# Kernel optimization log

Hardware: AMD Instinct MI355X
Metric: run time of the kernel (lower is better)

Reference implementation:

```python
import jax, jax.numpy as jnp
import numpy as np
import math

NH = 12      # num attention heads
WIN = 128    # one-sided sliding window
NG = 32      # number of global (prefix) tokens
NEG = -1e9
LN_EPS = 1e-12


def _layernorm(x, g, b):
    mu = jnp.mean(x, axis=-1, keepdims=True)
    var = jnp.mean(jnp.square(x - mu), axis=-1, keepdims=True)
    return (x - mu) * jax.lax.rsqrt(var + LN_EPS) * g + b


def _longformer_self_attn(h, am, Wq, bq, Wk, bk, Wv, bv):
    B, S, D = h.shape
    Dh = D // NH
    w = WIN
    C = S // w  # number of chunks

    def proj(Wm, bm):
        return (h @ Wm + bm).reshape(B, S, NH, Dh).transpose(0, 2, 1, 3)

    q = proj(Wq, bq) * (1.0 / math.sqrt(Dh))  # [B,H,S,Dh]
    k = proj(Wk, bk)
    v = proj(Wv, bv)

    # ---- banded (sliding window) scores, chunked: each query chunk sees 3w keys ----
    kp = jnp.pad(k, ((0, 0), (0, 0), (w, w), (0, 0)))
    vp = jnp.pad(v, ((0, 0), (0, 0), (w, w), (0, 0)))
    idx = jnp.arange(C)[:, None] * w + jnp.arange(3 * w)[None, :]  # [C,3w]
    k3 = kp[:, :, idx]  # [B,H,C,3w,Dh]
    v3 = vp[:, :, idx]
    qc = q.reshape(B, NH, C, w, Dh)
    band = jnp.einsum('bhcqd,bhckd->bhcqk', qc, k3)  # [B,H,C,w,3w]

    qpos = (jnp.arange(C) * w)[:, None, None] + jnp.arange(w)[None, :, None]  # [C,w,1]
    kpos = (idx - w)[:, None, :]  # [C,1,3w] absolute key positions
    valid = (jnp.abs(kpos - qpos) <= w) & (kpos >= NG) & (kpos < S)  # band, exclude global keys

    amp = jnp.pad(am, ((0, 0), (w, w)))
    am3 = amp[:, idx]  # [B,C,3w] additive mask gathered per chunk
    band = band + am3[:, None, :, None, :]
    band = jnp.where(valid[None, None], band, NEG)
    band = band.reshape(B, NH, S, 3 * w)

    # ---- every token also attends to the NG global tokens ----
    gsc = jnp.einsum('bhsd,bhgd->bhsg', q, k[:, :, :NG]) + am[:, None, None, :NG]

    logits = jnp.concatenate([band, gsc], axis=-1)  # [B,H,S,3w+NG]
    probs = jax.nn.softmax(logits, axis=-1)
    pb = probs[..., :3 * w].reshape(B, NH, C, w, 3 * w)
    out = jnp.einsum('bhcqk,bhckd->bhcqd', pb, v3).reshape(B, NH, S, Dh)
    out = out + jnp.einsum('bhsg,bhgd->bhsd', probs[..., 3 * w:], v[:, :, :NG])

    # ---- global tokens attend to everything ----
    gl = jnp.einsum('bhgd,bhsd->bhgs', q[:, :, :NG], k) + am[:, None, None, :]
    outg = jnp.einsum('bhgs,bhsd->bhgd', jax.nn.softmax(gl, axis=-1), v)

    ctx = jnp.concatenate([outg, out[:, :, NG:]], axis=2)  # [B,H,S,Dh]
    return ctx.transpose(0, 2, 1, 3).reshape(B, S, D)


def setup_inputs() -> dict:
    key = jax.random.key(0)
    ks = jax.random.split(key, 8)
    B, S, D, F = 2, 4096, 768, 3072
    p = lambda k_, sh: jax.random.normal(k_, sh, jnp.float32) * 0.02
    return {
        'hidden_states': jax.random.normal(ks[0], (B, S, D), jnp.float32),
        'attention_mask': jnp.zeros((B, S), jnp.float32),
        'Wq': p(ks[1], (D, D)), 'bq': jnp.zeros((D,), jnp.float32),
        'Wk': p(ks[2], (D, D)), 'bk': jnp.zeros((D,), jnp.float32),
        'Wv': p(ks[3], (D, D)), 'bv': jnp.zeros((D,), jnp.float32),
        'Wo': p(ks[4], (D, D)), 'bo': jnp.zeros((D,), jnp.float32),
        'ln1_g': jnp.ones((D,), jnp.float32), 'ln1_b': jnp.zeros((D,), jnp.float32),
        'Wi': p(ks[5], (D, F)), 'bi': jnp.zeros((F,), jnp.float32),
        'Wo2': p(ks[6], (F, D)), 'bo2': jnp.zeros((D,), jnp.float32),
        'ln2_g': jnp.ones((D,), jnp.float32), 'ln2_b': jnp.zeros((D,), jnp.float32),
    }


def reference(hidden_states, attention_mask, Wq, bq, Wk, bk, Wv, bv, Wo, bo,
              ln1_g, ln1_b, Wi, bi, Wo2, bo2, ln2_g, ln2_b):
    ctx = _longformer_self_attn(hidden_states, attention_mask, Wq, bq, Wk, bk, Wv, bv)
    attn_out = _layernorm(ctx @ Wo + bo + hidden_states, ln1_g, ln1_b)
    inter = jax.nn.gelu(attn_out @ Wi + bi, approximate=False)
    layer_out = _layernorm(inter @ Wo2 + bo2 + attn_out, ln2_g, ln2_b)
    return layer_out
```

## Files before the change

kernel.cpp:

```cpp
#include <hip/hip_runtime.h>
#include <math.h>

#define NHEAD 12
#define DH 64
#define S_LEN 4096
#define B_SZ 2
#define D_MODEL 768
#define FF_DIM 3072
#define WINSZ 128
#define NGLB 32
#define NEGV -1e9f
#define NQC 6291456L

typedef __attribute__((ext_vector_type(8))) short bf16x8;
typedef __attribute__((ext_vector_type(4))) float floatx4;

__device__ __forceinline__ unsigned short f2bf(float x) {
    union { float f; unsigned u; } v; v.f = x;
    unsigned r = v.u + 0x7fffu + ((v.u >> 16) & 1u);
    return (unsigned short)(r >> 16);
}
__device__ __forceinline__ float bf2f(unsigned short x) {
    union { unsigned u; float f; } v; v.u = ((unsigned)x) << 16;
    return v.f;
}

__device__ __forceinline__ void async_copy16(const unsigned short* g, unsigned short* l) {
    __builtin_amdgcn_global_load_lds(
        (const __attribute__((address_space(1))) void*)g,
        (__attribute__((address_space(3))) void*)l, 16, 0, 0);
}

__global__ __launch_bounds__(256) void conv_k(
    const float* __restrict__ x, unsigned short* __restrict__ y, long n)
{
    long i = ((long)blockIdx.x * 256 + threadIdx.x) * 4;
    if (i >= n) return;
    float4 v = *(const float4*)(x + i);
    ushort4 o;
    o.x = f2bf(v.x); o.y = f2bf(v.y); o.z = f2bf(v.z); o.w = f2bf(v.w);
    *(ushort4*)(y + i) = o;
}

__global__ __launch_bounds__(256) void bcat_k(
    const float* __restrict__ a, const float* __restrict__ b,
    const float* __restrict__ c, float* __restrict__ o)
{
    int i = blockIdx.x * 256 + threadIdx.x;
    if (i < 768) o[i] = a[i];
    else if (i < 1536) o[i] = b[i - 768];
    else if (i < 2304) o[i] = c[i - 1536];
}

__global__ __launch_bounds__(256) void transpose_k(
    const float* __restrict__ W, unsigned short* __restrict__ WT, int K, int N)
{
    __shared__ float tile[32][33];
    const int tx = threadIdx.x, ty = threadIdx.y;
    const int n0 = blockIdx.x * 32, k0 = blockIdx.y * 32;
#pragma unroll
    for (int i = 0; i < 4; ++i)
        tile[ty + 8 * i][tx] = W[(long)(k0 + ty + 8 * i) * N + n0 + tx];
    __syncthreads();
#pragma unroll
    for (int i = 0; i < 4; ++i)
        WT[(long)(n0 + ty + 8 * i) * K + k0 + tx] = f2bf(tile[tx][ty + 8 * i]);
}

__global__ __launch_bounds__(256) void vt_k(
    const unsigned short* __restrict__ v, unsigned short* __restrict__ vt)
{
    const int bh = blockIdx.y;
    const int s0 = blockIdx.x * 32;
    const int w = threadIdx.x >> 6, lane = threadIdx.x & 63;
    const unsigned short* src = v + ((long)bh * S_LEN + s0 + w * 8) * DH + lane;
    unsigned short r[8];
#pragma unroll
    for (int j = 0; j < 8; ++j) r[j] = src[j * DH];
    unsigned short* dst = vt + ((long)bh * DH + lane) * S_LEN + s0 + w * 8;
    ushort4 lo, hi;
    lo.x = r[0]; lo.y = r[1]; lo.z = r[2]; lo.w = r[3];
    hi.x = r[4]; hi.y = r[5]; hi.z = r[6]; hi.w = r[7];
    *(ushort4*)dst = lo;
    *(ushort4*)(dst + 4) = hi;
}

template <int EPI>
__global__ __launch_bounds__(256) void gemm_bf(
    const unsigned short* __restrict__ A, const unsigned short* __restrict__ BT,
    const float* __restrict__ bias, void* __restrict__ out,
    int M, int N, int K, int nx)
{
    __shared__ unsigned short As[128 * 32];
    __shared__ unsigned short Bs[128 * 32];
    const int tid = threadIdx.x;
    const int wave = tid >> 6, lane = tid & 63;
    const int t8 = (blockIdx.x & 7) * (gridDim.x >> 3) + (blockIdx.x >> 3);
    const int m0 = (t8 / nx) * 128, n0 = (t8 % nx) * 128;
    const int wr = (wave >> 1) * 64, wc = (wave & 1) * 64;

    floatx4 acc[4][4];
#pragma unroll
    for (int i = 0; i < 4; ++i)
#pragma unroll
        for (int j = 0; j < 4; ++j) acc[i][j] = (floatx4){0.f, 0.f, 0.f, 0.f};

    const int srow = lane >> 2;
    const int schk = (((lane & 3) ^ (srow & 3))) * 8;
    const int r = lane & 15;
    const int q8 = ((lane >> 4) ^ (lane & 3)) * 8;

    for (int k0 = 0; k0 < K; k0 += 32) {
#pragma unroll
        for (int gi = 0; gi < 2; ++gi) {
            const int g = wave * 2 + gi;
            async_copy16(A + (long)(m0 + g * 16 + srow) * K + k0 + schk, &As[g * 512]);
            async_copy16(BT + (long)(n0 + g * 16 + srow) * K + k0 + schk, &Bs[g * 512]);
        }
        __syncthreads();

        bf16x8 af[4], bfr[4];
#pragma unroll
        for (int i = 0; i < 4; ++i) {
            af[i]  = *(const bf16x8*)&As[(wr + i * 16 + r) * 32 + q8];
            bfr[i] = *(const bf16x8*)&Bs[(wc + i * 16 + r) * 32 + q8];
        }
#pragma unroll
        for (int i = 0; i < 4; ++i)
#pragma unroll
            for (int j = 0; j < 4; ++j)
                acc[i][j] = __builtin_amdgcn_mfma_f32_16x16x32_bf16(
                    af[i], bfr[j], acc[i][j], 0, 0, 0);
        __syncthreads();
    }

    const int col_l = lane & 15, row_l = (lane >> 4) * 4;
#pragma unroll
    for (int i = 0; i < 4; ++i) {
#pragma unroll
        for (int j = 0; j < 4; ++j) {
            const int n = n0 + wc + j * 16 + col_l;
            const float bv = bias[n];
#pragma unroll
            for (int rg = 0; rg < 4; ++rg) {
                const int m = m0 + wr + i * 16 + row_l + rg;
                float v = acc[i][j][rg] + bv;
                if (EPI == 1) {
                    v = 0.5f * v * (1.f + erff(v * 0.70710678118654752f));
                    ((unsigned short*)out)[(long)m * N + n] = f2bf(v);
                } else {
                    const int bb = m >> 12, s = m & 4095;
                    const int part = n / 768;
                    const int nn = n - part * 768;
                    const int hh = nn >> 6, dh = nn & 63;
                    const float sc = (part == 0) ? 0.125f : 1.f;
                    ((unsigned short*)out)[(long)part * NQC +
                        (((long)bb * NHEAD + hh) * S_LEN + s) * DH + dh] = f2bf(v * sc);
                }
            }
        }
    }
}

__global__ __launch_bounds__(256) void gemm_sp(
    const unsigned short* __restrict__ A, const unsigned short* __restrict__ BT,
    float* __restrict__ p0, float* __restrict__ p1,
    int M, int N, int K2, int nx, int ntile)
{
    __shared__ unsigned short As[128 * 32];
    __shared__ unsigned short Bs[128 * 32];
    const int tid = threadIdx.x;
    const int wave = tid >> 6, lane = tid & 63;
    const int t8 = (blockIdx.x & 7) * (gridDim.x >> 3) + (blockIdx.x >> 3);
    const int slice = t8 >= ntile;
    const int tile = t8 - slice * ntile;
    const int m0 = (tile / nx) * 128, n0 = (tile % nx) * 128;
    const int kbeg = slice * K2, kend = kbeg + K2;
    float* P = slice ? p1 : p0;
    const int wr = (wave >> 1) * 64, wc = (wave & 1) * 64;

    floatx4 acc[4][4];
#pragma unroll
    for (int i = 0; i < 4; ++i)
#pragma unroll
        for (int j = 0; j < 4; ++j) acc[i][j] = (floatx4){0.f, 0.f, 0.f, 0.f};

    const int srow = lane >> 2;
    const int schk = (((lane & 3) ^ (srow & 3))) * 8;
    const int r = lane & 15;
    const int q8 = ((lane >> 4) ^ (lane & 3)) * 8;
    const long Kl = (long)K2 * 2;

    for (int k0 = kbeg; k0 < kend; k0 += 32) {
#pragma unroll
        for (int gi = 0; gi < 2; ++gi) {
            const int g = wave * 2 + gi;
            async_copy16(A + (long)(m0 + g * 16 + srow) * Kl + k0 + schk, &As[g * 512]);
            async_copy16(BT + (long)(n0 + g * 16 + srow) * Kl + k0 + schk, &Bs[g * 512]);
        }
        __syncthreads();

        bf16x8 af[4], bfr[4];
#pragma unroll
        for (int i = 0; i < 4; ++i) {
            af[i]  = *(const bf16x8*)&As[(wr + i * 16 + r) * 32 + q8];
            bfr[i] = *(const bf16x8*)&Bs[(wc + i * 16 + r) * 32 + q8];
        }
#pragma unroll
        for (int i = 0; i < 4; ++i)
#pragma unroll
            for (int j = 0; j < 4; ++j)
                acc[i][j] = __builtin_amdgcn_mfma_f32_16x16x32_bf16(
                    af[i], bfr[j], acc[i][j], 0, 0, 0);
        __syncthreads();
    }

    const int col_l = lane & 15, row_l = (lane >> 4) * 4;
#pragma unroll
    for (int i = 0; i < 4; ++i)
#pragma unroll
        for (int j = 0; j < 4; ++j) {
            const int n = n0 + wc + j * 16 + col_l;
#pragma unroll
            for (int rg = 0; rg < 4; ++rg) {
                const int m = m0 + wr + i * 16 + row_l + rg;
                P[(long)m * N + n] = acc[i][j][rg];
            }
        }
}

__global__ __launch_bounds__(256) void band_mfma_k(
    const unsigned short* __restrict__ q, const unsigned short* __restrict__ k,
    const unsigned short* __restrict__ vt, const float* __restrict__ am,
    unsigned short* __restrict__ ctx)
{
    __shared__ unsigned short Ks[32 * 72];
    __shared__ unsigned short Vs[64 * 40];
    __shared__ unsigned short Ps[4][32 * 40];

    const int blk = blockIdx.x;
    const int c = blk & 31;
    const int h = (blk >> 5) % NHEAD;
    const int b = blk / (32 * NHEAD);
    const int tid = threadIdx.x;
    const int wave = tid >> 6, lane = tid & 63;
    const long bh = (long)b * NHEAD + h;

    const unsigned short* kh  = k + bh * S_LEN * DH;
    const unsigned short* vth = vt + bh * (long)DH * S_LEN;
    const float* amb = am + (long)b * S_LEN;

    const int q0 = c * WINSZ + wave * 32;
    const int ln15 = lane & 15, ln4 = lane >> 4;

    bf16x8 qf[2][2];
#pragma unroll
    for (int nt = 0; nt < 2; ++nt)
#pragma unroll
        for (int ks = 0; ks < 2; ++ks)
            qf[nt][ks] = *(const bf16x8*)(q + (bh * S_LEN + q0 + nt * 16 + ln15) * DH
                                          + ks * 32 + ln4 * 8);

    floatx4 o[4][2];
#pragma unroll
    for (int mt = 0; mt < 4; ++mt)
#pragma unroll
        for (int nt = 0; nt < 2; ++nt) o[mt][nt] = (floatx4){0.f, 0.f, 0.f, 0.f};
    float m_r[2] = {-1e30f, -1e30f}, l_r[2] = {0.f, 0.f};

    const int sk_key = tid >> 3, sk_ch = tid & 7;
    const int sv_dim = tid & 63, sv_ch = tid >> 6;
    const bf16x8 zero8 = {0, 0, 0, 0, 0, 0, 0, 0};

    for (int tile = 0; tile < 13; ++tile) {
        const bool glob = (tile == 12);
        const int kbase = glob ? 0 : (c * WINSZ - WINSZ + tile * 32);

        __syncthreads();
        {
            int kpos = kbase + sk_key;
            bf16x8 val = zero8;
            if ((unsigned)kpos < (unsigned)S_LEN)
                val = *(const bf16x8*)(kh + (long)kpos * DH + sk_ch * 8);
            *(bf16x8*)(&Ks[sk_key * 72 + sk_ch * 8]) = val;
        }
        {
            int kc = kbase + sv_ch * 8;
            bf16x8 val = zero8;
            if (kc >= 0 && kc + 8 <= S_LEN)
                val = *(const bf16x8*)(vth + (long)sv_dim * S_LEN + kc);
            *(bf16x8*)(&Vs[sv_dim * 40 + sv_ch * 8]) = val;
        }
        __syncthreads();

        bf16x8 ak[2][2];
#pragma unroll
        for (int mt = 0; mt < 2; ++mt)
#pragma unroll
            for (int ks = 0; ks < 2; ++ks)
                ak[mt][ks] = *(const bf16x8*)(&Ks[(mt * 16 + ln15) * 72 + ks * 32 + ln4 * 8]);

        floatx4 s[2][2];
#pragma unroll
        for (int mt = 0; mt < 2; ++mt)
#pragma unroll
            for (int nt = 0; nt < 2; ++nt) {
                floatx4 acc = (floatx4){0.f, 0.f, 0.f, 0.f};
                acc = __builtin_amdgcn_mfma_f32_16x16x32_bf16(ak[mt][0], qf[nt][0], acc, 0, 0, 0);
                acc = __builtin_amdgcn_mfma_f32_16x16x32_bf16(ak[mt][1], qf[nt][1], acc, 0, 0, 0);
                s[mt][nt] = acc;
            }

#pragma unroll
        for (int mt = 0; mt < 2; ++mt) {
            const int kp0 = kbase + mt * 16 + ln4 * 4;
#pragma unroll
            for (int rg = 0; rg < 4; ++rg) {
                const int kpos = kp0 + rg;
                const bool kin = (unsigned)kpos < (unsigned)S_LEN;
                const float amv = kin ? amb[kpos] : 0.f;
#pragma unroll
                for (int nt = 0; nt < 2; ++nt) {
                    const int qpos = q0 + nt * 16 + ln15;
                    const int dlt = kpos > qpos ? kpos - qpos : qpos - kpos;
                    const bool valid = glob || (kpos >= NGLB && kin && dlt <= WINSZ);
                    s[mt][nt][rg] = valid ? s[mt][nt][rg] + amv : NEGV;
                }
            }
        }

        float alpha[2];
#pragma unroll
        for (int nt = 0; nt < 2; ++nt) {
            float mx = s[0][nt][0];
#pragma unroll
            for (int rg = 1; rg < 4; ++rg) mx = fmaxf(mx, s[0][nt][rg]);
#pragma unroll
            for (int rg = 0; rg < 4; ++rg) mx = fmaxf(mx, s[1][nt][rg]);
            mx = fmaxf(mx, __shfl_xor(mx, 16));
            mx = fmaxf(mx, __shfl_xor(mx, 32));
            const float mn = fmaxf(m_r[nt], mx);
            alpha[nt] = __expf(m_r[nt] - mn);
            m_r[nt] = mn;
        }

#pragma unroll
        for (int nt = 0; nt < 2; ++nt) {
            float sum = 0.f;
#pragma unroll
            for (int mt = 0; mt < 2; ++mt) {
                ushort4 pk;
#pragma unroll
                for (int rg = 0; rg < 4; ++rg) {
                    const float p = __expf(s[mt][nt][rg] - m_r[nt]);
                    sum += p;
                    ((unsigned short*)&pk)[rg] = f2bf(p);
                }
                *(ushort4*)(&Ps[wave][(nt * 16 + ln15) * 40 + mt * 16 + ln4 * 4]) = pk;
            }
            sum += __shfl_xor(sum, 16);
            sum += __shfl_xor(sum, 32);
            l_r[nt] = l_r[nt] * alpha[nt] + sum;
        }

#pragma unroll
        for (int mt = 0; mt < 4; ++mt)
#pragma unroll
            for (int nt = 0; nt < 2; ++nt)
#pragma unroll
                for (int rg = 0; rg < 4; ++rg) o[mt][nt][rg] *= alpha[nt];

        bf16x8 av[4], bp[2];
#pragma unroll
        for (int mt = 0; mt < 4; ++mt)
            av[mt] = *(const bf16x8*)(&Vs[(mt * 16 + ln15) * 40 + ln4 * 8]);
#pragma unroll
        for (int nt = 0; nt < 2; ++nt)
            bp[nt] = *(const bf16x8*)(&Ps[wave][(nt * 16 + ln15) * 40 + ln4 * 8]);
#pragma unroll
        for (int mt = 0; mt < 4; ++mt)
#pragma unroll
            for (int nt = 0; nt < 2; ++nt)
                o[mt][nt] = __builtin_amdgcn_mfma_f32_16x16x32_bf16(
                    av[mt], bp[nt], o[mt][nt], 0, 0, 0);
    }

    const float inv0 = 1.f / l_r[0], inv1 = 1.f / l_r[1];
#pragma unroll
    for (int nt = 0; nt < 2; ++nt) {
        const float inv = nt ? inv1 : inv0;
        const long row = (long)b * S_LEN + q0 + nt * 16 + ln15;
#pragma unroll
        for (int mt = 0; mt < 4; ++mt) {
            ushort4 ov;
#pragma unroll
            for (int rg = 0; rg < 4; ++rg)
                ((unsigned short*)&ov)[rg] = f2bf(o[mt][nt][rg] * inv);
            *(ushort4*)(ctx + row * D_MODEL + h * DH + mt * 16 + ln4 * 4) = ov;
        }
    }
}

__global__ __launch_bounds__(512) void glob_mfma_k(
    const unsigned short* __restrict__ q, const unsigned short* __restrict__ k,
    const unsigned short* __restrict__ vt, const float* __restrict__ am,
    unsigned short* __restrict__ ctx)
{
    __shared__ unsigned short Ps[8][32 * 72];
    __shared__ float Om[64 * 36];
    __shared__ float mW[8][32], lW[8][32], lTot[32];

    const int bh = blockIdx.x;
    const int b = bh / NHEAD, h = bh % NHEAD;
    const int tid = threadIdx.x;
    const int wave = tid >> 6, lane = tid & 63;
    const int ln15 = lane & 15, ln4 = lane >> 4;

    const unsigned short* kh  = k + (long)bh * S_LEN * DH;
    const unsigned short* vth = vt + (long)bh * DH * S_LEN;
    const float* amb = am + (long)b * S_LEN;

    bf16x8 qf[2][2];
#pragma unroll
    for (int nt = 0; nt < 2; ++nt)
#pragma unroll
        for (int ks = 0; ks < 2; ++ks)
            qf[nt][ks] = *(const bf16x8*)(q + ((long)bh * S_LEN + nt * 16 + ln15) * DH
                                          + ks * 32 + ln4 * 8);

    floatx4 o[4][2];
#pragma unroll
    for (int mt = 0; mt < 4; ++mt)
#pragma unroll
        for (int nt = 0; nt < 2; ++nt) o[mt][nt] = (floatx4){0.f, 0.f, 0.f, 0.f};
    float m_r[2] = {-1e30f, -1e30f}, l_r[2] = {0.f, 0.f};

    for (int it = 0; it < 8; ++it) {
        const int kbase = it * 512 + wave * 64;

        bf16x8 ak[4][2];
#pragma unroll
        for (int mt = 0; mt < 4; ++mt)
#pragma unroll
            for (int ks = 0; ks < 2; ++ks)
                ak[mt][ks] = *(const bf16x8*)(kh + (long)(kbase + mt * 16 + ln15) * DH
                                              + ks * 32 + ln4 * 8);

        floatx4 s[4][2];
#pragma unroll
        for (int mt = 0; mt < 4; ++mt)
#pragma unroll
            for (int nt = 0; nt < 2; ++nt) {
                floatx4 acc = (floatx4){0.f, 0.f, 0.f, 0.f};
                acc = __builtin_amdgcn_mfma_f32_16x16x32_bf16(ak[mt][0], qf[nt][0], acc, 0, 0, 0);
                acc = __builtin_amdgcn_mfma_f32_16x16x32_bf16(ak[mt][1], qf[nt][1], acc, 0, 0, 0);
                s[mt][nt] = acc;
            }

#pragma unroll
        for (int mt = 0; mt < 4; ++mt) {
            const int kp0 = kbase + mt * 16 + ln4 * 4;
#pragma unroll
            for (int rg = 0; rg < 4; ++rg) {
                const float amv = amb[kp0 + rg];
#pragma unroll
                for (int nt = 0; nt < 2; ++nt) s[mt][nt][rg] += amv;
            }
        }

        float alpha[2];
#pragma unroll
        for (int nt = 0; nt < 2; ++nt) {
            float mx = s[0][nt][0];
#pragma unroll
            for (int mt = 0; mt < 4; ++mt)
#pragma unroll
                for (int rg = 0; rg < 4; ++rg) mx = fmaxf(mx, s[mt][nt][rg]);
            mx = fmaxf(mx, __shfl_xor(mx, 16));
            mx = fmaxf(mx, __shfl_xor(mx, 32));
            const float mn = fmaxf(m_r[nt], mx);
            alpha[nt] = __expf(m_r[nt] - mn);
            m_r[nt] = mn;
        }

#pragma unroll
        for (int nt = 0; nt < 2; ++nt) {
            float sum = 0.f;
#pragma unroll
            for (int mt = 0; mt < 4; ++mt) {
                ushort4 pk;
#pragma unroll
                for (int rg = 0; rg < 4; ++rg) {
                    const float p = __expf(s[mt][nt][rg] - m_r[nt]);
                    sum += p;
                    ((unsigned short*)&pk)[rg] = f2bf(p);
                }
                *(ushort4*)(&Ps[wave][(nt * 16 + ln15) * 72 + mt * 16 + ln4 * 4]) = pk;
            }
            sum += __shfl_xor(sum, 16);
            sum += __shfl_xor(sum, 32);
            l_r[nt] = l_r[nt] * alpha[nt] + sum;
        }

#pragma unroll
        for (int mt = 0; mt < 4; ++mt)
#pragma unroll
            for (int nt = 0; nt < 2; ++nt)
#pragma unroll
                for (int rg = 0; rg < 4; ++rg) o[mt][nt][rg] *= alpha[nt];

        bf16x8 av[4][2], bp[2][2];
#pragma unroll
        for (int mt = 0; mt < 4; ++mt)
#pragma unroll
            for (int ks = 0; ks < 2; ++ks)
                av[mt][ks] = *(const bf16x8*)(vth + (long)(mt * 16 + ln15) * S_LEN
                                              + kbase + ks * 32 + ln4 * 8);
#pragma unroll
        for (int nt = 0; nt < 2; ++nt)
#pragma unroll
            for (int ks = 0; ks < 2; ++ks)
                bp[nt][ks] = *(const bf16x8*)(&Ps[wave][(nt * 16 + ln15) * 72
                                              + ks * 32 + ln4 * 8]);
#pragma unroll
        for (int mt = 0; mt < 4; ++mt)
#pragma unroll
            for (int nt = 0; nt < 2; ++nt) {
                o[mt][nt] = __builtin_amdgcn_mfma_f32_16x16x32_bf16(
                    av[mt][0], bp[nt][0], o[mt][nt], 0, 0, 0);
                o[mt][nt] = __builtin_amdgcn_mfma_f32_16x16x32_bf16(
                    av[mt][1], bp[nt][1], o[mt][nt], 0, 0, 0);
            }
    }

    if (ln4 == 0) {
#pragma unroll
        for (int nt = 0; nt < 2; ++nt) {
            mW[wave][nt * 16 + ln15] = m_r[nt];
            lW[wave][nt * 16 + ln15] = l_r[nt];
        }
    }
    for (int i = tid; i < 64 * 36; i += 512) Om[i] = 0.f;
    __syncthreads();

    float f[2];
#pragma unroll
    for (int nt = 0; nt < 2; ++nt) {
        const int qq = nt * 16 + ln15;
        float mt_ = mW[0][qq];
#pragma unroll
        for (int w = 1; w < 8; ++w) mt_ = fmaxf(mt_, mW[w][qq]);
        float lt = 0.f;
#pragma unroll
        for (int w = 0; w < 8; ++w) lt += __expf(mW[w][qq] - mt_) * lW[w][qq];
        f[nt] = __expf(m_r[nt] - mt_);
        if (wave == 0 && ln4 == 0) lTot[qq] = lt;
    }
#pragma unroll
    for (int mt = 0; mt < 4; ++mt)
#pragma unroll
        for (int nt = 0; nt < 2; ++nt)
#pragma unroll
            for (int rg = 0; rg < 4; ++rg) o[mt][nt][rg] *= f[nt];

    for (int wv = 0; wv < 8; ++wv) {
        if (wave == wv) {
#pragma unroll
            for (int mt = 0; mt < 4; ++mt)
#pragma unroll
                for (int nt = 0; nt < 2; ++nt)
#pragma unroll
                    for (int rg = 0; rg < 4; ++rg)
                        Om[(mt * 16 + ln4 * 4 + rg) * 36 + nt * 16 + ln15] += o[mt][nt][rg];
        }
        __syncthreads();
    }

    const int qq = tid >> 4, d0 = (tid & 15) * 4;
    const float inv = 1.f / lTot[qq];
    ushort4 ov;
#pragma unroll
    for (int i = 0; i < 4; ++i)
        ((unsigned short*)&ov)[i] = f2bf(Om[(d0 + i) * 36 + qq] * inv);
    *(ushort4*)(ctx + ((long)b * S_LEN + qq) * D_MODEL + h * DH + d0) = ov;
}

__global__ __launch_bounds__(256) void ln2p_k(
    const float* __restrict__ p0, const float* __restrict__ p1,
    const float* __restrict__ bias, const float* __restrict__ resid,
    float* __restrict__ out, unsigned short* __restrict__ out_bf,
    const float* __restrict__ gw, const float* __restrict__ bw)
{
    __shared__ float red[256];
    const long row = blockIdx.x;
    const long base = row * D_MODEL;
    const int t = threadIdx.x;
    float v0 = p0[base + t]       + p1[base + t]       + bias[t]       + resid[base + t];
    float v1 = p0[base + t + 256] + p1[base + t + 256] + bias[t + 256] + resid[base + t + 256];
    float v2 = p0[base + t + 512] + p1[base + t + 512] + bias[t + 512] + resid[base + t + 512];

    red[t] = v0 + v1 + v2;
    __syncthreads();
    for (int off = 128; off; off >>= 1) {
        if (t < off) red[t] += red[t + off];
        __syncthreads();
    }
    const float mu = red[0] * (1.f / 768.f);
    __syncthreads();

    float d0 = v0 - mu, d1 = v1 - mu, d2 = v2 - mu;
    red[t] = d0 * d0 + d1 * d1 + d2 * d2;
    __syncthreads();
    for (int off = 128; off; off >>= 1) {
        if (t < off) red[t] += red[t + off];
        __syncthreads();
    }
    const float var = red[0] * (1.f / 768.f);
    const float rs = rsqrtf(var + 1e-12f);

    const float y0 = d0 * rs * gw[t] + bw[t];
    const float y1 = d1 * rs * gw[t + 256] + bw[t + 256];
    const float y2 = d2 * rs * gw[t + 512] + bw[t + 512];
    if (out) {
        float* y = out + base;
        y[t] = y0; y[t + 256] = y1; y[t + 512] = y2;
    }
    if (out_bf) {
        unsigned short* yb = out_bf + base;
        yb[t] = f2bf(y0); yb[t + 256] = f2bf(y1); yb[t + 512] = f2bf(y2);
    }
}

extern "C" void kernel_launch(void* const* d_in, const int* in_sizes, int n_in,
                              void* d_out, int out_size, void* d_ws, size_t ws_size,
                              hipStream_t stream)
{
    const float* hid  = (const float*)d_in[0];
    const float* am   = (const float*)d_in[1];
    const float* Wq   = (const float*)d_in[2];
    const float* bq   = (const float*)d_in[3];
    const float* Wk   = (const float*)d_in[4];
    const float* bk   = (const float*)d_in[5];
    const float* Wv   = (const float*)d_in[6];
    const float* bv   = (const float*)d_in[7];
    const float* Wo   = (const float*)d_in[8];
    const float* bo   = (const float*)d_in[9];
    const float* ln1g = (const float*)d_in[10];
    const float* ln1b = (const float*)d_in[11];
    const float* Wi   = (const float*)d_in[12];
    const float* bi   = (const float*)d_in[13];
    const float* Wo2  = (const float*)d_in[14];
    const float* bo2  = (const float*)d_in[15];
    const float* ln2g = (const float*)d_in[16];
    const float* ln2b = (const float*)d_in[17];

    const long M  = (long)B_SZ * S_LEN;
    const long NQ = NQC;

    unsigned short* W16 = (unsigned short*)d_ws;
    unsigned short* qb   = W16;
    unsigned short* kb   = W16 + NQ;
    unsigned short* vb   = W16 + 2 * NQ;
    unsigned short* vtb  = W16 + 3 * NQ;
    unsigned short* ctxb = W16 + 4 * NQ;
    unsigned short* hidb = W16 + 5 * NQ;
    unsigned short* wqt  = W16 + 6 * NQ;
    unsigned short* wkt  = wqt + 589824;
    unsigned short* wvt  = wkt + 589824;
    unsigned short* wot  = wvt + 589824;
    unsigned short* wit  = wot + 589824;
    unsigned short* wo2t = wit + 2359296;
    float* tmp   = (float*)(W16 + 44826624);
    float* partB1 = (float*)(W16 + 57409536);
    float* bcat  = (float*)(W16 + 69992448);
    float* partA0 = (float*)W16;
    float* partA1 = (float*)(W16 + 2 * NQ);
    unsigned short* interb = W16;
    unsigned short* attnb  = hidb;
    float* partB0 = (float*)(W16 + 4 * NQ);
    (void)ws_size; (void)in_sizes; (void)n_in; (void)out_size;

    transpose_k<<<dim3(24, 24), dim3(32, 8), 0, stream>>>(Wq, wqt, 768, 768);
    transpose_k<<<dim3(24, 24), dim3(32, 8), 0, stream>>>(Wk, wkt, 768, 768);
    transpose_k<<<dim3(24, 24), dim3(32, 8), 0, stream>>>(Wv, wvt, 768, 768);
    transpose_k<<<dim3(24, 24), dim3(32, 8), 0, stream>>>(Wo, wot, 768, 768);
    transpose_k<<<dim3(96, 24), dim3(32, 8), 0, stream>>>(Wi, wit, 768, 3072);
    transpose_k<<<dim3(24, 96), dim3(32, 8), 0, stream>>>(Wo2, wo2t, 3072, 768);
    conv_k<<<dim3((NQ / 4 + 255) / 256), dim3(256), 0, stream>>>(hid, hidb, NQ);
    bcat_k<<<dim3(9), dim3(256), 0, stream>>>(bq, bk, bv, bcat);

    dim3 blk(256);

    gemm_bf<2><<<dim3(1152), blk, 0, stream>>>(hidb, wqt, bcat, qb,
                                               M, 2304, 768, 18);

    vt_k<<<dim3(128, 24), blk, 0, stream>>>(vb, vtb);

    band_mfma_k<<<dim3(768), blk, 0, stream>>>(qb, kb, vtb, am, ctxb);
    glob_mfma_k<<<dim3(B_SZ * NHEAD), dim3(512), 0, stream>>>(qb, kb, vtb, am, ctxb);

    gemm_sp<<<dim3(768), blk, 0, stream>>>(ctxb, wot, partA0, partA1,
                                           M, 768, 384, 6, 384);
    ln2p_k<<<dim3(M), blk, 0, stream>>>(partA0, partA1, bo, hid,
                                        tmp, attnb, ln1g, ln1b);

    gemm_bf<1><<<dim3(1536), blk, 0, stream>>>(attnb, wit, bi, interb,
                                               M, 3072, 768, 24);

    gemm_sp<<<dim3(768), blk, 0, stream>>>(interb, wo2t, partB0, partB1,
                                           M, 768, 1536, 6, 384);
    ln2p_k<<<dim3(M), blk, 0, stream>>>(partB0, partB1, bo2, tmp,
                                        (float*)d_out, nullptr, ln2g, ln2b);
}
```

Measured before the change: 462.9 us.

## Replace GEMMs with 256x256-tile 8-wave double-buffered pipelined MFMA kernel

Replaces the 128x128, single-buffered 4-wave GEMM kernels (gemm_bf and gemm_sp) with one templated 512-thread kernel. It computes 256x256 tiles with a K step of 64 and double-buffers shared memory, issuing async copies for the next tile while MFMA runs. It also adds explicit barriers, waitcnt, sched_barrier and setprio scheduling. The aim is more data reuse per tile and latency hiding in the QKV, output, FFN1 and FFN2 GEMMs. In exchange, 128KB of LDS and large accumulators limit occupancy, and grids become small (192-384 blocks), which risks poor CU utilization on 256 CUs.

```diff
diff --git a/kernel.cpp b/kernel.cpp
--- a/kernel.cpp
+++ b/kernel.cpp
@@ -85,148 +85,188 @@
     *(ushort4*)(dst + 4) = hi;
 }
 
+#define MFMA_QUAD(MM, NN, BREG)                                                \
+    __builtin_amdgcn_s_setprio(1);                                             \
+    _Pragma("unroll")                                                          \
+    for (int f = 0; f < 4; ++f)                                                \
+        _Pragma("unroll")                                                      \
+        for (int g = 0; g < 2; ++g)                                            \
+            _Pragma("unroll")                                                  \
+            for (int ks = 0; ks < 2; ++ks)                                     \
+                acc[(MM) * 4 + f][(NN) * 2 + g] =                              \
+                    __builtin_amdgcn_mfma_f32_16x16x32_bf16(                   \
+                        af[f][ks], BREG[g][ks], acc[(MM) * 4 + f][(NN) * 2 + g], 0, 0, 0); \
+    __builtin_amdgcn_s_setprio(0);
+
 template <int EPI>
-__global__ __launch_bounds__(256) void gemm_bf(
+__global__ __launch_bounds__(512, 2) void gemm8(
     const unsigned short* __restrict__ A, const unsigned short* __restrict__ BT,
-    const float* __restrict__ bias, void* __restrict__ out,
-    int M, int N, int K, int nx)
-{
-    __shared__ unsigned short As[128 * 32];
-    __shared__ unsigned short Bs[128 * 32];
+    const float* __restrict__ bias, void* __restrict__ out, float* __restrict__ out1,
+    int M, int N, int Kst, int K2, int nx, int ntile)
+{
+    __shared__ __align__(16) unsigned short As[32768];
+    __shared__ __align__(16) unsigned short Bs[32768];
+
     const int tid = threadIdx.x;
-    const int wave = tid >> 6, lane = tid & 63;
-    const int t8 = (blockIdx.x & 7) * (gridDim.x >> 3) + (blockIdx.x >> 3);
-    const int m0 = (t8 / nx) * 128, n0 = (t8 % nx) * 128;
-    const int wr = (wave >> 1) * 64, wc = (wave & 1) * 64;
-
-    floatx4 acc[4][4];
-#pragma unroll
-    for (int i = 0; i < 4; ++i)
+    const int w = tid >> 6, lane = tid & 63;
+    int t8 = (blockIdx.x & 7) * (gridDim.x >> 3) + (blockIdx.x >> 3);
+    int kbeg = 0;
+    float* P = (float*)out;
+    if (EPI == 0) {
+        if (t8 >= ntile) { t8 -= ntile; kbeg = K2; P = out1; }
+    }
+    const int m0 = (t8 / nx) * 256, n0 = (t8 % nx) * 256;
+    const int NT = K2 >> 6;
+
+    const int wr = w >> 2, wc = w & 3;
+    const int ln15 = lane & 15, ln4 = lane >> 4;
+    const int wr8 = wr << 3, wc4 = wc << 2;
+
+    const int srow = lane >> 2;
+    const int scol = ((lane & 3) << 3) ^ ((lane & 32) >> 1);
+    const int ruA = w * 16 + srow;
+    const int rA0 = ((ruA >> 6) << 7) + (ruA & 63);
+    const int rB0 = ((ruA >> 5) << 6) + (ruA & 31);
+    const unsigned short* gA[2];
+    const unsigned short* gB[2];
+    gA[0] = A + (long)(m0 + rA0) * Kst + kbeg + scol;
+    gA[1] = A + (long)(m0 + rA0 + 64) * Kst + kbeg + scol;
+    gB[0] = BT + (long)(n0 + rB0) * Kst + kbeg + scol;
+    gB[1] = BT + (long)(n0 + rB0 + 32) * Kst + kbeg + scol;
+    const int wld = w << 10;
+
+    auto issueA = [&](int mu, int tt) {
+        const unsigned short* g = gA[mu] + (long)tt * 64;
+        unsigned short* l = &As[((((tt & 1) << 1) | mu) << 13) + wld];
+        async_copy16(g, l);
+        async_copy16(g + 32, l + 512);
+    };
+    auto issueB = [&](int nu, int tt) {
+        const unsigned short* g = gB[nu] + (long)tt * 64;
+        unsigned short* l = &Bs[((((tt & 1) << 1) | nu) << 13) + wld];
+        async_copy16(g, l);
+        async_copy16(g + 32, l + 512);
+    };
+
+    const int p2 = ((ln15 << 5) | (ln4 << 3)) ^ ((ln15 & 8) << 1);
+
+    floatx4 acc[8][4];
+#pragma unroll
+    for (int i = 0; i < 8; ++i)
 #pragma unroll
         for (int j = 0; j < 4; ++j) acc[i][j] = (floatx4){0.f, 0.f, 0.f, 0.f};
-
-    const int srow = lane >> 2;
-    const int schk = (((lane & 3) ^ (srow & 3))) * 8;
-    const int r = lane & 15;
-    const int q8 = ((lane >> 4) ^ (lane & 3)) * 8;
-
-    for (int k0 = 0; k0 < K; k0 += 32) {
-#pragma unroll
-        for (int gi = 0; gi < 2; ++gi) {
-            const int g = wave * 2 + gi;
-            async_copy16(A + (long)(m0 + g * 16 + srow) * K + k0 + schk, &As[g * 512]);
-            async_copy16(BT + (long)(n0 + g * 16 + srow) * K + k0 + schk, &Bs[g * 512]);
-        }
-        __syncthreads();
-
-        bf16x8 af[4], bfr[4];
-#pragma unroll
-        for (int i = 0; i < 4; ++i) {
-            af[i]  = *(const bf16x8*)&As[(wr + i * 16 + r) * 32 + q8];
-            bfr[i] = *(const bf16x8*)&Bs[(wc + i * 16 + r) * 32 + q8];
-        }
-#pragma unroll
-        for (int i = 0; i < 4; ++i)
-#pragma unroll
-            for (int j = 0; j < 4; ++j)
-                acc[i][j] = __builtin_amdgcn_mfma_f32_16x16x32_bf16(
-                    af[i], bfr[j], acc[i][j], 0, 0, 0);
-        __syncthreads();
-    }
-
-    const int col_l = lane & 15, row_l = (lane >> 4) * 4;
-#pragma unroll
-    for (int i = 0; i < 4; ++i) {
-#pragma unroll
-        for (int j = 0; j < 4; ++j) {
-            const int n = n0 + wc + j * 16 + col_l;
-            const float bv = bias[n];
-#pragma unroll
-            for (int rg = 0; rg < 4; ++rg) {
-                const int m = m0 + wr + i * 16 + row_l + rg;
-                float v = acc[i][j][rg] + bv;
-                if (EPI == 1) {
+    bf16x8 af[4][2], b0[2][2], b1[2][2];
+
+    issueA(0, 0); issueB(0, 0); issueA(1, 0); issueB(1, 0);
+    if (NT > 1) {
+        issueA(0, 1); issueB(0, 1);
+        asm volatile("s_waitcnt vmcnt(4)" ::: "memory");
+    } else {
+        asm volatile("s_waitcnt vmcnt(0)" ::: "memory");
+    }
+    __builtin_amdgcn_s_barrier();
+    __builtin_amdgcn_sched_barrier(0);
+
+    for (int u = 0; u < NT; ++u) {
+        const unsigned short* Ab = &As[((u & 1) << 14) + p2];
+        const unsigned short* Bb = &Bs[((u & 1) << 14) + p2];
+
+#pragma unroll
+        for (int f = 0; f < 4; ++f)
+#pragma unroll
+            for (int ks = 0; ks < 2; ++ks)
+                af[f][ks] = *(const bf16x8*)(Ab + ((wr8 + f * 2 + ks) << 9));
+#pragma unroll
+        for (int g = 0; g < 2; ++g)
+#pragma unroll
+            for (int ks = 0; ks < 2; ++ks)
+                b0[g][ks] = *(const bf16x8*)(Bb + ((wc4 + g * 2 + ks) << 9));
+        if (u + 1 < NT) issueA(1, u + 1);
+        __builtin_amdgcn_sched_barrier(0);
+        __builtin_amdgcn_s_barrier();
+        asm volatile("s_waitcnt lgkmcnt(0)" ::: "memory");
+        __builtin_amdgcn_sched_barrier(0);
+        MFMA_QUAD(0, 0, b0)
+        __builtin_amdgcn_sched_barrier(0);
+        __builtin_amdgcn_s_barrier();
+
+#pragma unroll
+        for (int g = 0; g < 2; ++g)
+#pragma unroll
+            for (int ks = 0; ks < 2; ++ks)
+                b1[g][ks] = *(const bf16x8*)(Bb + 8192 + ((wc4 + g * 2 + ks) << 9));
+        if (u + 1 < NT) issueB(1, u + 1);
+        __builtin_amdgcn_sched_barrier(0);
+        __builtin_amdgcn_s_barrier();
+        asm volatile("s_waitcnt lgkmcnt(0)" ::: "memory");
+        __builtin_amdgcn_sched_barrier(0);
+        MFMA_QUAD(0, 1, b1)
+        __builtin_amdgcn_sched_barrier(0);
+        __builtin_amdgcn_s_barrier();
+
+#pragma unroll
+        for (int f = 0; f < 4; ++f)
+#pragma unroll
+            for (int ks = 0; ks < 2; ++ks)
+                af[f][ks] = *(const bf16x8*)(Ab + 8192 + ((wr8 + f * 2 + ks) << 9));
+        if (u + 2 < NT) issueA(0, u + 2);
+        __builtin_amdgcn_sched_barrier(0);
+        __builtin_amdgcn_s_barrier();
+        asm volatile("s_waitcnt lgkmcnt(0)" ::: "memory");
+        __builtin_amdgcn_sched_barrier(0);
+        MFMA_QUAD(1, 0, b0)
+        __builtin_amdgcn_sched_barrier(0);
+        __builtin_amdgcn_s_barrier();
+
+        if (u + 2 < NT) issueB(0, u + 2);
+        __builtin_amdgcn_sched_barrier(0);
+        __builtin_amdgcn_s_barrier();
+        asm volatile("s_waitcnt lgkmcnt(0)" ::: "memory");
+        __builtin_amdgcn_sched_barrier(0);
+        MFMA_QUAD(1, 1, b1)
+        __builtin_amdgcn_sched_barrier(0);
+        if (u + 2 < NT)      asm volatile("s_waitcnt vmcnt(4)" ::: "memory");
+        else if (u + 1 < NT) asm volatile("s_waitcnt vmcnt(0)" ::: "memory");
+        __builtin_amdgcn_s_barrier();
+        __builtin_amdgcn_sched_barrier(0);
+    }
+
+    const int col_l = lane & 15, row_l = ln4 << 2;
+#pragma unroll
+    for (int mi = 0; mi < 8; ++mi) {
+        const int mbase = m0 + wr * 128 + ((mi >> 2) << 6) + ((mi & 3) << 4) + row_l;
+#pragma unroll
+        for (int ni = 0; ni < 4; ++ni) {
+            const int n = n0 + wc * 64 + ((ni >> 1) << 5) + ((ni & 1) << 4) + col_l;
+            if (EPI == 0) {
+#pragma unroll
+                for (int rg = 0; rg < 4; ++rg)
+                    P[(long)(mbase + rg) * N + n] = acc[mi][ni][rg];
+            } else if (EPI == 1) {
+                const float bv = bias[n];
+#pragma unroll
+                for (int rg = 0; rg < 4; ++rg) {
+                    float v = acc[mi][ni][rg] + bv;
                     v = 0.5f * v * (1.f + erff(v * 0.70710678118654752f));
-                    ((unsigned short*)out)[(long)m * N + n] = f2bf(v);
-                } else {
+                    ((unsigned short*)out)[(long)(mbase + rg) * N + n] = f2bf(v);
+                }
+            } else {
+                const float bv = bias[n];
+                const int part = n / 768;
+                const int nn = n - part * 768;
+                const int hh = nn >> 6, dh = nn & 63;
+                const float sc = (part == 0) ? 0.125f : 1.f;
+#pragma unroll
+                for (int rg = 0; rg < 4; ++rg) {
+                    const int m = mbase + rg;
                     const int bb = m >> 12, s = m & 4095;
-                    const int part = n / 768;
-                    const int nn = n - part * 768;
-                    const int hh = nn >> 6, dh = nn & 63;
-                    const float sc = (part == 0) ? 0.125f : 1.f;
                     ((unsigned short*)out)[(long)part * NQC +
-                        (((long)bb * NHEAD + hh) * S_LEN + s) * DH + dh] = f2bf(v * sc);
+                        (((long)bb * NHEAD + hh) * S_LEN + s) * DH + dh] =
+                        f2bf((acc[mi][ni][rg] + bv) * sc);
                 }
             }
         }
     }
-}
-
-__global__ __launch_bounds__(256) void gemm_sp(
-    const unsigned short* __restrict__ A, const unsigned short* __restrict__ BT,
-    float* __restrict__ p0, float* __restrict__ p1,
-    int M, int N, int K2, int nx, int ntile)
-{
-    __shared__ unsigned short As[128 * 32];
-    __shared__ unsigned short Bs[128 * 32];
-    const int tid = threadIdx.x;
-    const int wave = tid >> 6, lane = tid & 63;
-    const int t8 = (blockIdx.x & 7) * (gridDim.x >> 3) + (blockIdx.x >> 3);
-    const int slice = t8 >= ntile;
-    const int tile = t8 - slice * ntile;
-    const int m0 = (tile / nx) * 128, n0 = (tile % nx) * 128;
-    const int kbeg = slice * K2, kend = kbeg + K2;
-    float* P = slice ? p1 : p0;
-    const int wr = (wave >> 1) * 64, wc = (wave & 1) * 64;
-
-    floatx4 acc[4][4];
-#pragma unroll
-    for (int i = 0; i < 4; ++i)
-#pragma unroll
-        for (int j = 0; j < 4; ++j) acc[i][j] = (floatx4){0.f, 0.f, 0.f, 0.f};
-
-    const int srow = lane >> 2;
-    const int schk = (((lane & 3) ^ (srow & 3))) * 8;
-    const int r = lane & 15;
-    const int q8 = ((lane >> 4) ^ (lane & 3)) * 8;
-    const long Kl = (long)K2 * 2;
-
-    for (int k0 = kbeg; k0 < kend; k0 += 32) {
-#pragma unroll
-        for (int gi = 0; gi < 2; ++gi) {
-            const int g = wave * 2 + gi;
-            async_copy16(A + (long)(m0 + g * 16 + srow) * Kl + k0 + schk, &As[g * 512]);
-            async_copy16(BT + (long)(n0 + g * 16 + srow) * Kl + k0 + schk, &Bs[g * 512]);
-        }
-        __syncthreads();
-
-        bf16x8 af[4], bfr[4];
-#pragma unroll
-        for (int i = 0; i < 4; ++i) {
-            af[i]  = *(const bf16x8*)&As[(wr + i * 16 + r) * 32 + q8];
-            bfr[i] = *(const bf16x8*)&Bs[(wc + i * 16 + r) * 32 + q8];
-        }
-#pragma unroll
-        for (int i = 0; i < 4; ++i)
-#pragma unroll
-            for (int j = 0; j < 4; ++j)
-                acc[i][j] = __builtin_amdgcn_mfma_f32_16x16x32_bf16(
-                    af[i], bfr[j], acc[i][j], 0, 0, 0);
-        __syncthreads();
-    }
-
-    const int col_l = lane & 15, row_l = (lane >> 4) * 4;
-#pragma unroll
-    for (int i = 0; i < 4; ++i)
-#pragma unroll
-        for (int j = 0; j < 4; ++j) {
-            const int n = n0 + wc + j * 16 + col_l;
-#pragma unroll
-            for (int rg = 0; rg < 4; ++rg) {
-                const int m = m0 + wr + i * 16 + row_l + rg;
-                P[(long)m * N + n] = acc[i][j][rg];
-            }
-        }
 }
 
 __global__ __launch_bounds__(256) void band_mfma_k(
@@ -689,26 +729,24 @@
     conv_k<<<dim3((NQ / 4 + 255) / 256), dim3(256), 0, stream>>>(hid, hidb, NQ);
     bcat_k<<<dim3(9), dim3(256), 0, stream>>>(bq, bk, bv, bcat);
 
-    dim3 blk(256);
-
-    gemm_bf<2><<<dim3(1152), blk, 0, stream>>>(hidb, wqt, bcat, qb,
-                                               M, 2304, 768, 18);
-
-    vt_k<<<dim3(128, 24), blk, 0, stream>>>(vb, vtb);
-
-    band_mfma_k<<<dim3(768), blk, 0, stream>>>(qb, kb, vtb, am, ctxb);
+    gemm8<2><<<dim3(288), dim3(512), 0, stream>>>(hidb, wqt, bcat, qb, nullptr,
+                                                  (int)M, 2304, 768, 768, 9, 0);
+
+    vt_k<<<dim3(128, 24), dim3(256), 0, stream>>>(vb, vtb);
+
+    band_mfma_k<<<dim3(768), dim3(256), 0, stream>>>(qb, kb, vtb, am, ctxb);
     glob_mfma_k<<<dim3(B_SZ * NHEAD), dim3(512), 0, stream>>>(qb, kb, vtb, am, ctxb);
 
-    gemm_sp<<<dim3(768), blk, 0, stream>>>(ctxb, wot, partA0, partA1,
-                                           M, 768, 384, 6, 384);
-    ln2p_k<<<dim3(M), blk, 0, stream>>>(partA0, partA1, bo, hid,
-                                        tmp, attnb, ln1g, ln1b);
-
-    gemm_bf<1><<<dim3(1536), blk, 0, stream>>>(attnb, wit, bi, interb,
-                                               M, 3072, 768, 24);
-
-    gemm_sp<<<dim3(768), blk, 0, stream>>>(interb, wo2t, partB0, partB1,
-                                           M, 768, 1536, 6, 384);
-    ln2p_k<<<dim3(M), blk, 0, stream>>>(partB0, partB1, bo2, tmp,
-                                        (float*)d_out, nullptr, ln2g, ln2b);
-}
+    gemm8<0><<<dim3(192), dim3(512), 0, stream>>>(ctxb, wot, nullptr, partA0, partA1,
+                                                  (int)M, 768, 768, 384, 3, 96);
+    ln2p_k<<<dim3(M), dim3(256), 0, stream>>>(partA0, partA1, bo, hid,
+                                              tmp, attnb, ln1g, ln1b);
+
+    gemm8<1><<<dim3(384), dim3(512), 0, stream>>>(attnb, wit, bi, interb, nullptr,
+                                                  (int)M, 3072, 768, 768, 12, 0);
+
+    gemm8<0><<<dim3(192), dim3(512), 0, stream>>>(interb, wo2t, nullptr, partB0, partB1,
+                                                  (int)M, 768, 3072, 1536, 3, 96);
+    ln2p_k<<<dim3(M), dim3(256), 0, stream>>>(partB0, partB1, bo2, tmp,
+                                              (float*)d_out, nullptr, ln2g, ln2b);
+}
```

After: 475.9 us. +2.8%, slower.
